# Kernel tuning notes

Hardware: AMD Instinct MI355X
Metric: run time of the kernel (lower is better)

## Reference

```python
import jax, jax.numpy as jnp
import numpy as np

FEATURE_MAPS = [38, 19, 10, 5, 3, 1]
NUM_ANCHORS = [4, 6, 6, 6, 4, 4]
SCALE_RANGE = (0.1, 0.9)
RATIO_RANGE = (0.5, 2.0)
BACKGROUND_ID = 0
EPS = 1e-6


def make_anchors():
    # Replicates AnchorManager._generate_anchors: for each level, loop i (rows -> cy),
    # j (cols -> cx), then zip(scales, ratios) anchor shapes. Returns [A, 4] cxcywh.
    all_a = []
    for size, na in zip(FEATURE_MAPS, NUM_ANCHORS):
        scales = np.linspace(SCALE_RANGE[0], SCALE_RANGE[1], na)
        ratios = np.linspace(RATIO_RANGE[0], RATIO_RANGE[1], na)
        rs = np.sqrt(ratios)
        w = scales * rs
        h = scales / rs
        c = (np.arange(size) + 0.5) / size
        cy_g, cx_g = np.meshgrid(c, c, indexing='ij')  # i -> cy, j -> cx
        centers = np.stack([cx_g.ravel(), cy_g.ravel()], axis=-1)  # [size*size, 2]
        wh = np.stack([w, h], axis=-1)  # [na, 2]
        a = np.concatenate([np.repeat(centers, na, axis=0), np.tile(wh, (size * size, 1))], axis=1)
        all_a.append(a)
    return np.concatenate(all_a).astype(np.float32)  # [8732, 4]


def _cxcywh_to_xyxy(b):
    return jnp.concatenate([b[..., :2] - b[..., 2:] * 0.5, b[..., :2] + b[..., 2:] * 0.5], axis=-1)


def _pairwise_iou(a, b):
    # a: [B, A, 4] xyxy, b: [B, N, 4] xyxy -> [B, A, N]
    lt = jnp.maximum(a[:, :, None, :2], b[:, None, :, :2])
    rb = jnp.minimum(a[:, :, None, 2:], b[:, None, :, 2:])
    wh = jnp.clip(rb - lt, 0.0)
    inter = wh[..., 0] * wh[..., 1]
    area_a = (a[..., 2] - a[..., 0]) * (a[..., 3] - a[..., 1])
    area_b = (b[..., 2] - b[..., 0]) * (b[..., 3] - b[..., 1])
    union = area_a[:, :, None] + area_b[:, None, :] - inter
    return inter / jnp.maximum(union, EPS)


def setup_inputs() -> dict:
    key = jax.random.key(0)
    k1, k2 = jax.random.split(key)
    B, N = 32, 100
    gt_boxes = jax.random.uniform(k1, (B, N, 4), dtype=jnp.float32)
    gt_labels = jax.random.randint(k2, (B, N), 0, 81, dtype=jnp.int32)
    mask = jnp.ones((B, N), dtype=bool)
    anchors = jnp.asarray(make_anchors())
    return {"gt_boxes": gt_boxes, "gt_labels": gt_labels, "mask": mask, "anchors": anchors}


def reference(gt_boxes, gt_labels, mask, anchors):
    B, N, _ = gt_boxes.shape
    A = anchors.shape[0]
    anc = jnp.broadcast_to(anchors, (B, A, 4))
    anc_xyxy = _cxcywh_to_xyxy(anc)
    ious = _pairwise_iou(anc_xyxy, gt_boxes)  # [B, A, N]

    best_gt_iou = ious.max(axis=-1)          # [B, A]
    best_gt_idx = ious.argmax(axis=-1)       # [B, A]
    best_anchor_idx = ious.argmax(axis=-2)   # [B, N]

    bidx = jnp.arange(B)[:, None]
    best_gt_idx = best_gt_idx.at[bidx, best_anchor_idx].set(jnp.broadcast_to(jnp.arange(N), (B, N)))
    best_gt_iou = best_gt_iou.at[bidx, best_anchor_idx].set(2.0)

    pos_mask = best_gt_iou > 0.5  # [B, A]

    matched_gtb = jnp.take_along_axis(gt_boxes, best_gt_idx[..., None], axis=1)  # [B, A, 4]
    matched_lab = jnp.take_along_axis(gt_labels, best_gt_idx, axis=1)           # [B, A]

    ex = (matched_gtb[..., 0] - anc[..., 0]) / anc[..., 2]
    ey = (matched_gtb[..., 1] - anc[..., 1]) / anc[..., 3]
    ew = jnp.log((matched_gtb[..., 2] + EPS) / (anc[..., 2] + EPS))
    eh = jnp.log((matched_gtb[..., 3] + EPS) / (anc[..., 3] + EPS))
    encoded = jnp.stack([ex, ey, ew, eh], axis=-1)  # [B, A, 4]

    encoded_labels = jnp.where(pos_mask, matched_lab, jnp.int32(BACKGROUND_ID))

    # Batches with no valid GT keep zeros / background (the `continue` branch)
    any_valid = mask.any(axis=-1)  # [B]
    encoded = jnp.where(any_valid[:, None, None], encoded, 0.0)
    encoded_labels = jnp.where(any_valid[:, None], encoded_labels, jnp.int32(BACKGROUND_ID))
    return encoded, encoded_labels, pos_mask
```

## Files before the change

### kernel.cpp

```cpp
#include <hip/hip_runtime.h>

#define A_ 8732
#define B_ 32
#define N_ 100
#define ABLK 35
#define GB_G 4
#define GMAX 25
#define SPLIT 8
#define SLEN 1092
#define EPSF 1e-6f


__global__ __launch_bounds__(256) void k_pre(
    const float* __restrict__ gt, float4* __restrict__ cbox,
    float* __restrict__ carea, int* __restrict__ cn, int* __restrict__ cnt) {
  __shared__ int s_cnt[B_];
  int tid = threadIdx.x;
  if (tid < B_) s_cnt[tid] = 0;
  __syncthreads();
  for (int j = tid; j < B_ * N_; j += 256) {
    float4 gb = ((const float4*)gt)[j];
    if (gb.z > gb.x && gb.w > gb.y) {
      int b = j / N_;
      int p = atomicAdd(&s_cnt[b], 1);
      cbox[b * N_ + p] = gb;
      carea[b * N_ + p] = (gb.z - gb.x) * (gb.w - gb.y);
      cn[b * N_ + p] = j - b * N_;
    }
  }
  __syncthreads();
  if (tid < B_) cnt[tid] = s_cnt[tid];
}

__global__ __launch_bounds__(256) void k_scan(
    const float* __restrict__ anchors, const float4* __restrict__ cbox,
    const float* __restrict__ carea, const int* __restrict__ cn,
    const int* __restrict__ cnt, unsigned long long* __restrict__ partial,
    unsigned long long* __restrict__ wsplit) {
  int tid = threadIdx.x;
  int bid = blockIdx.x;
  int s = bid % SPLIT;
  int t = bid / SPLIT;
  int g = t % GMAX;
  int b = t / GMAX;
  int c = cnt[b];
  if (GB_G * g >= c) return;
  __shared__ unsigned long long sred[256];

  float gx0[GB_G], gy0[GB_G], gx1[GB_G], gy1[GB_G], gar[GB_G];
  int gn[GB_G];
  bool live[GB_G];
#pragma unroll
  for (int j = 0; j < GB_G; j++) {
    int p = GB_G * g + j;
    live[j] = p < c;
    int ps = live[j] ? p : 0;
    float4 gb = cbox[b * N_ + ps];
    if (!live[j]) gb = make_float4(1.0f, 1.0f, 0.0f, 0.0f);
    gx0[j] = gb.x; gy0[j] = gb.y; gx1[j] = gb.z; gy1[j] = gb.w;
    gar[j] = carea[b * N_ + ps];
    gn[j] = live[j] ? cn[b * N_ + ps] : 0;
  }

  int s0 = s * SLEN;
  int send = (s0 + SLEN < A_) ? (s0 + SLEN) : A_;

  unsigned long long wkey[GB_G];
#pragma unroll
  for (int j = 0; j < GB_G; j++)
    wkey[j] = (unsigned long long)(0xFFFFFFFFu - (unsigned)(s0 + tid));

  unsigned long long* prow = partial + ((size_t)b * GMAX + g) * A_;
  for (int a = s0 + tid; a < send; a += 256) {
    float4 an = ((const float4*)anchors)[a];
    float ax0 = an.x - an.z * 0.5f, ay0 = an.y - an.w * 0.5f;
    float ax1 = an.x + an.z * 0.5f, ay1 = an.y + an.w * 0.5f;
    float area_a = (ax1 - ax0) * (ay1 - ay0);
    unsigned long long pk = 0ull;
#pragma unroll
    for (int j = 0; j < GB_G; j++) {
      float lx = fmaxf(ax0, gx0[j]), ly = fmaxf(ay0, gy0[j]);
      float rx = fminf(ax1, gx1[j]), ry = fminf(ay1, gy1[j]);
      float w = fmaxf(rx - lx, 0.0f), h = fmaxf(ry - ly, 0.0f);
      float inter = w * h;
      if (inter > 0.0f) {
        float uni = area_a + gar[j] - inter;
        float iou = inter / fmaxf(uni, EPSF);
        unsigned long long hi = ((unsigned long long)__float_as_uint(iou)) << 32;
        unsigned long long kA = hi | (unsigned long long)(unsigned)(N_ - 1 - gn[j]);
        if (kA > pk) pk = kA;
        unsigned long long kB = hi | (unsigned long long)(0xFFFFFFFFu - (unsigned)a);
        if (kB > wkey[j]) wkey[j] = kB;
      }
    }
    prow[a] = pk;
  }

#pragma unroll
  for (int j = 0; j < GB_G; j++) {
    sred[tid] = wkey[j];
    __syncthreads();
    for (int r = 128; r > 0; r >>= 1) {
      if (tid < r) {
        unsigned long long o = sred[tid + r];
        if (o > sred[tid]) sred[tid] = o;
      }
      __syncthreads();
    }
    if (tid == 0 && live[j])
      wsplit[((size_t)b * SPLIT + s) * N_ + gn[j]] = sred[0];
    __syncthreads();
  }
}

__global__ __launch_bounds__(256) void k_finalize(
    const float* __restrict__ gt, const int* __restrict__ labels,
    const float* __restrict__ anchors, const unsigned char* __restrict__ mask,
    const unsigned long long* __restrict__ partial,
    const unsigned long long* __restrict__ wsplit,
    const int* __restrict__ cnt, float* __restrict__ out) {
  int b = blockIdx.y;
  int a0 = blockIdx.x * 256;
  int tid = threadIdx.x;
  int a = a0 + tid;

  __shared__ int s_ov[256];
  __shared__ int s_any;
  if (tid == 0) s_any = 0;
  s_ov[tid] = -1;
  __syncthreads();
  if (tid < N_) {
    float4 gb = ((const float4*)gt)[b * N_ + tid];
    int aw = 0;
    if (gb.z > gb.x && gb.w > gb.y) {
      const unsigned long long* wp = wsplit + (size_t)b * SPLIT * N_ + tid;
      unsigned long long k = wp[0];
#pragma unroll
      for (int s2 = 1; s2 < SPLIT; s2++) {
        unsigned long long tk = wp[(size_t)s2 * N_];
        if (tk > k) k = tk;
      }
      aw = (int)(0xFFFFFFFFu - (unsigned)(k & 0xFFFFFFFFull));
    }
    if (aw >= a0 && aw < a0 + 256) atomicMax(&s_ov[aw - a0], tid);
  }
  if (tid < 25) {
    unsigned v = ((const unsigned*)mask)[b * 25 + tid];
    if (v) atomicOr(&s_any, 1);
  }
  __syncthreads();
  if (a >= A_) return;

  int G = (cnt[b] + GB_G - 1) / GB_G;
  unsigned long long k = (unsigned long long)(unsigned)(N_ - 1);
  const unsigned long long* prow = partial + (size_t)b * GMAX * A_ + a;
  for (int g2 = 0; g2 < G; g2++) {
    unsigned long long t2 = prow[(size_t)g2 * A_];
    if (t2 > k) k = t2;
  }
  float iou = __uint_as_float((unsigned)(k >> 32));
  int gi = (N_ - 1) - (int)(k & 0xFFFFFFFFull);

  int ov = s_ov[tid];
  bool pos;
  if (ov >= 0) {
    gi = ov;
    pos = true;
  } else {
    pos = iou > 0.5f;
  }

  float4 an = ((const float4*)anchors)[a];
  const float* g = gt + (size_t)(b * N_ + gi) * 4;
  float gx = g[0], gy = g[1], gw = g[2], gh = g[3];

  float ex = (gx - an.x) / an.z;
  float ey = (gy - an.y) / an.w;
  float ew = logf((gw + EPSF) / (an.z + EPSF));
  float eh = logf((gh + EPSF) / (an.w + EPSF));
  int lab = pos ? labels[b * N_ + gi] : 0;

  if (!s_any) { ex = 0.0f; ey = 0.0f; ew = 0.0f; eh = 0.0f; lab = 0; }

  const long long BA = (long long)B_ * A_;
  ((float4*)out)[(size_t)b * A_ + a] = make_float4(ex, ey, ew, eh);
  out[4 * BA + (size_t)b * A_ + a] = (float)lab;
  out[5 * BA + (size_t)b * A_ + a] = pos ? 1.0f : 0.0f;
}

extern "C" void kernel_launch(void* const* d_in, const int* in_sizes, int n_in,
                              void* d_out, int out_size, void* d_ws,
                              size_t ws_size, hipStream_t stream) {
  const float* gt = (const float*)d_in[0];
  const int* labels = (const int*)d_in[1];
  const unsigned char* mask = (const unsigned char*)d_in[2];
  const float* anchors = (const float*)d_in[3];
  float* out = (float*)d_out;

  unsigned long long* partial = (unsigned long long*)d_ws;
  unsigned long long* wsplit = partial + (size_t)B_ * GMAX * A_;
  float4* cbox = (float4*)(wsplit + (size_t)B_ * SPLIT * N_);
  float* carea = (float*)(cbox + B_ * N_);
  int* cn = (int*)(carea + B_ * N_);
  int* cnt = cn + B_ * N_;

  k_pre<<<1, 256, 0, stream>>>(gt, cbox, carea, cn, cnt);
  k_scan<<<B_ * GMAX * SPLIT, 256, 0, stream>>>(anchors, cbox, carea, cn, cnt,
                                                partial, wsplit);
  k_finalize<<<dim3(ABLK, B_), 256, 0, stream>>>(gt, labels, anchors, mask,
                                                 partial, wsplit, cnt, out);
}
```

Baseline: 87.36 us.

## Fold GT compaction into scan kernel via ballot and use wave-shuffle reductions

```diff
diff --git a/kernel.cpp b/kernel.cpp
--- a/kernel.cpp
+++ b/kernel.cpp
@@ -11,41 +11,40 @@
 #define EPSF 1e-6f
 
 
-__global__ __launch_bounds__(256) void k_pre(
-    const float* __restrict__ gt, float4* __restrict__ cbox,
-    float* __restrict__ carea, int* __restrict__ cn, int* __restrict__ cnt) {
-  __shared__ int s_cnt[B_];
-  int tid = threadIdx.x;
-  if (tid < B_) s_cnt[tid] = 0;
-  __syncthreads();
-  for (int j = tid; j < B_ * N_; j += 256) {
-    float4 gb = ((const float4*)gt)[j];
-    if (gb.z > gb.x && gb.w > gb.y) {
-      int b = j / N_;
-      int p = atomicAdd(&s_cnt[b], 1);
-      cbox[b * N_ + p] = gb;
-      carea[b * N_ + p] = (gb.z - gb.x) * (gb.w - gb.y);
-      cn[b * N_ + p] = j - b * N_;
-    }
-  }
-  __syncthreads();
-  if (tid < B_) cnt[tid] = s_cnt[tid];
-}
 
 __global__ __launch_bounds__(256) void k_scan(
-    const float* __restrict__ anchors, const float4* __restrict__ cbox,
-    const float* __restrict__ carea, const int* __restrict__ cn,
-    const int* __restrict__ cnt, unsigned long long* __restrict__ partial,
+    const float* __restrict__ gt, const float* __restrict__ anchors,
+    unsigned long long* __restrict__ partial,
     unsigned long long* __restrict__ wsplit) {
   int tid = threadIdx.x;
+  int lane = tid & 63, wid = tid >> 6;
   int bid = blockIdx.x;
   int s = bid % SPLIT;
   int t = bid / SPLIT;
   int g = t % GMAX;
   int b = t / GMAX;
-  int c = cnt[b];
+
+  __shared__ unsigned long long s_bal[2];
+  __shared__ int s_slot[N_];
+  __shared__ unsigned long long s_w[4][GB_G];
+
+  bool v = false;
+  float4 myg;
+  if (tid < N_) {
+    myg = ((const float4*)gt)[b * N_ + tid];
+    v = (myg.z > myg.x && myg.w > myg.y);
+  }
+  unsigned long long bal = __ballot(v);
+  if (lane == 0 && wid < 2) s_bal[wid] = bal;
+  __syncthreads();
+  int c0 = __popcll(s_bal[0]);
+  int c = c0 + __popcll(s_bal[1]);
+  if (v) {
+    int rank = __popcll(bal & ((1ull << lane) - 1)) + (wid ? c0 : 0);
+    s_slot[rank] = tid;
+  }
+  __syncthreads();
   if (GB_G * g >= c) return;
-  __shared__ unsigned long long sred[256];
 
   float gx0[GB_G], gy0[GB_G], gx1[GB_G], gy1[GB_G], gar[GB_G];
   int gn[GB_G];
@@ -54,12 +53,12 @@
   for (int j = 0; j < GB_G; j++) {
     int p = GB_G * g + j;
     live[j] = p < c;
-    int ps = live[j] ? p : 0;
-    float4 gb = cbox[b * N_ + ps];
+    int nj = live[j] ? s_slot[p] : 0;
+    gn[j] = nj;
+    float4 gb = ((const float4*)gt)[b * N_ + nj];
     if (!live[j]) gb = make_float4(1.0f, 1.0f, 0.0f, 0.0f);
     gx0[j] = gb.x; gy0[j] = gb.y; gx1[j] = gb.z; gy1[j] = gb.w;
-    gar[j] = carea[b * N_ + ps];
-    gn[j] = live[j] ? cn[b * N_ + ps] : 0;
+    gar[j] = (gb.z - gb.x) * (gb.w - gb.y);
   }
 
   int s0 = s * SLEN;
@@ -98,18 +97,24 @@
 
 #pragma unroll
   for (int j = 0; j < GB_G; j++) {
-    sred[tid] = wkey[j];
-    __syncthreads();
-    for (int r = 128; r > 0; r >>= 1) {
-      if (tid < r) {
-        unsigned long long o = sred[tid + r];
-        if (o > sred[tid]) sred[tid] = o;
-      }
-      __syncthreads();
-    }
-    if (tid == 0 && live[j])
-      wsplit[((size_t)b * SPLIT + s) * N_ + gn[j]] = sred[0];
-    __syncthreads();
+    unsigned long long k = wkey[j];
+#pragma unroll
+    for (int off = 32; off; off >>= 1) {
+      unsigned long long o = __shfl_xor(k, off, 64);
+      if (o > k) k = o;
+    }
+    if (lane == 0) s_w[wid][j] = k;
+  }
+  __syncthreads();
+  if (tid < GB_G) {
+    int j = tid;
+    if (GB_G * g + j < c) {
+      unsigned long long k = s_w[0][j];
+#pragma unroll
+      for (int w2 = 1; w2 < 4; w2++)
+        if (s_w[w2][j] > k) k = s_w[w2][j];
+      wsplit[((size_t)b * SPLIT + s) * N_ + s_slot[GB_G * g + j]] = k;
+    }
   }
 }
 
@@ -117,22 +122,32 @@
     const float* __restrict__ gt, const int* __restrict__ labels,
     const float* __restrict__ anchors, const unsigned char* __restrict__ mask,
     const unsigned long long* __restrict__ partial,
-    const unsigned long long* __restrict__ wsplit,
-    const int* __restrict__ cnt, float* __restrict__ out) {
+    const unsigned long long* __restrict__ wsplit, float* __restrict__ out) {
   int b = blockIdx.y;
   int a0 = blockIdx.x * 256;
   int tid = threadIdx.x;
+  int lane = tid & 63, wid = tid >> 6;
   int a = a0 + tid;
 
   __shared__ int s_ov[256];
   __shared__ int s_any;
+  __shared__ unsigned long long s_bal[2];
+
+  bool v = false;
+  if (tid < N_) {
+    float4 gb = ((const float4*)gt)[b * N_ + tid];
+    v = (gb.z > gb.x && gb.w > gb.y);
+  }
+  unsigned long long bal = __ballot(v);
+  if (lane == 0 && wid < 2) s_bal[wid] = bal;
   if (tid == 0) s_any = 0;
   s_ov[tid] = -1;
   __syncthreads();
+  int c = __popcll(s_bal[0]) + __popcll(s_bal[1]);
+
   if (tid < N_) {
-    float4 gb = ((const float4*)gt)[b * N_ + tid];
     int aw = 0;
-    if (gb.z > gb.x && gb.w > gb.y) {
+    if (v) {
       const unsigned long long* wp = wsplit + (size_t)b * SPLIT * N_ + tid;
       unsigned long long k = wp[0];
 #pragma unroll
@@ -145,13 +160,13 @@
     if (aw >= a0 && aw < a0 + 256) atomicMax(&s_ov[aw - a0], tid);
   }
   if (tid < 25) {
-    unsigned v = ((const unsigned*)mask)[b * 25 + tid];
-    if (v) atomicOr(&s_any, 1);
+    unsigned mv = ((const unsigned*)mask)[b * 25 + tid];
+    if (mv) atomicOr(&s_any, 1);
   }
   __syncthreads();
   if (a >= A_) return;
 
-  int G = (cnt[b] + GB_G - 1) / GB_G;
+  int G = (c + GB_G - 1) / GB_G;
   unsigned long long k = (unsigned long long)(unsigned)(N_ - 1);
   const unsigned long long* prow = partial + (size_t)b * GMAX * A_ + a;
   for (int g2 = 0; g2 < G; g2++) {
@@ -199,14 +214,8 @@
 
   unsigned long long* partial = (unsigned long long*)d_ws;
   unsigned long long* wsplit = partial + (size_t)B_ * GMAX * A_;
-  float4* cbox = (float4*)(wsplit + (size_t)B_ * SPLIT * N_);
-  float* carea = (float*)(cbox + B_ * N_);
-  int* cn = (int*)(carea + B_ * N_);
-  int* cnt = cn + B_ * N_;
-
-  k_pre<<<1, 256, 0, stream>>>(gt, cbox, carea, cn, cnt);
-  k_scan<<<B_ * GMAX * SPLIT, 256, 0, stream>>>(anchors, cbox, carea, cn, cnt,
-                                                partial, wsplit);
+
+  k_scan<<<B_ * GMAX * SPLIT, 256, 0, stream>>>(gt, anchors, partial, wsplit);
   k_finalize<<<dim3(ABLK, B_), 256, 0, stream>>>(gt, labels, anchors, mask,
-                                                 partial, wsplit, cnt, out);
+                                                 partial, wsplit, out);
 }
```

Result: faster. 82.50 us (median of 2 runs) (-5.6%).
